# Optimization experiments

Measured on AMD Instinct MI355X. Metric: run time of the kernel, lower is better.

## Reference

```python
import jax, jax.numpy as jnp
import numpy as np

B, D = 128, 16384
EPS = 0.05
MAX_DEPTH = 5
D_MAX = 1000.0


def setup_inputs() -> dict:
    key = jax.random.key(0)
    k1, k2 = jax.random.split(key)
    theta = jax.random.normal(k1, (B, D), dtype=jnp.float32)
    prec = jax.random.uniform(k2, (D,), dtype=jnp.float32)
    return {"theta": theta, "prec": prec}


def _energy(theta, prec):
    # per-chain potential energy U(theta): [B]
    return 0.5 * jnp.einsum('bd,d,bd->b', theta, prec, theta)


def _grad_energy(theta, prec):
    # mirrors torch autograd.grad(energy.sum(), theta)
    return jax.grad(lambda th: _energy(th, prec).sum())(theta)


def _bdot(a, b):
    return jnp.einsum('bd,bd->b', a, b)


def _leapfrog(theta, r, prec, eps):
    gU = _grad_energy(theta, prec)
    r = r - 0.5 * eps * gU
    theta = theta + eps * r
    e = _energy(theta, prec)
    gU = _grad_energy(theta, prec)
    r = r - 0.5 * eps * gU
    return theta, r, e


def _buildtree(theta, r, u, eps_dir, j, key, prec):
    # returns (theta_near, r_near, theta_far, r_far, theta_prop, n, s)
    if j == 0:
        th, rp, e = _leapfrog(theta, r, prec, eps_dir)
        H = e + 0.5 * _bdot(rp, rp)
        n_p = (u <= jnp.exp(-H)).astype(jnp.int32)
        s_p = (jnp.log(u) - D_MAX < -H).astype(jnp.int32)
        return th, rp, th, rp, th, n_p, s_p
    k1, k2, k3 = jax.random.split(key, 3)
    th_n, r_n, th_f, r_f, th_p, n_p, s_p = _buildtree(theta, r, u, eps_dir, j - 1, k1, prec)
    _, _, th_f2, r_f2, th_pp, n_pp, s_pp = _buildtree(th_f, r_f, u, eps_dir, j - 1, k2, prec)
    # accept proposal from second subtree with prob n'' / (n' + n''), masked by s'
    denom = jnp.maximum(n_p + n_pp, 1).astype(jnp.float32)
    flag = (jax.random.uniform(k3, n_p.shape) < n_pp.astype(jnp.float32) / denom) & (s_p >= 1)
    th_p = jnp.where(flag[:, None], th_pp, th_p)
    # u-turn check; v*(far - near) == theta_plus - theta_minus
    v = jnp.sign(eps_dir)
    d = th_f2 - th_n
    s_new = (s_p * s_pp
             * ((v * _bdot(d, r_n)) >= 0.0).astype(jnp.int32)
             * ((v * _bdot(d, r_f2)) >= 0.0).astype(jnp.int32))
    n_new = n_p + jnp.where(s_p >= 1, n_pp, 0)
    return th_n, r_n, th_f2, r_f2, th_p, n_new, s_new


def _sample_trajectory(theta0, prec, key):
    kr, ku, key = jax.random.split(key, 3)
    r0 = jax.random.normal(kr, theta0.shape, theta0.dtype)
    H0 = _energy(theta0, prec) + 0.5 * _bdot(r0, r0)
    u = jax.random.uniform(ku, H0.shape, theta0.dtype) * jnp.exp(-H0)
    theta_r = theta0
    theta_f = theta0
    r_r = r0
    r_f = r0
    theta_m = theta0
    n = jnp.ones((theta0.shape[0],), jnp.int32)
    s = jnp.ones((theta0.shape[0],), jnp.int32)
    for j in range(MAX_DEPTH):  # tree doubling, bounded depth (jit-friendly)
        key, kv, kt, ka = jax.random.split(key, 4)
        v = jnp.where(jax.random.normal(kv, ()) >= 0.0, 1.0, -1.0)
        neg = v < 0.0
        st_th = jnp.where(neg, theta_r, theta_f)
        st_r = jnp.where(neg, r_r, r_f)
        _, _, th_far, r_far, th_p, n_p, s_p = _buildtree(st_th, st_r, u, v * EPS, j, kt, prec)
        theta_r = jnp.where(neg, th_far, theta_r)
        r_r = jnp.where(neg, r_far, r_r)
        theta_f = jnp.where(neg, theta_f, th_far)
        r_f = jnp.where(neg, r_f, r_far)
        acc = jax.random.uniform(ka, n.shape) < jnp.minimum(
            n_p.astype(jnp.float32) / n.astype(jnp.float32), 1.0)
        acc = acc & (s >= 1) & (s_p >= 1)
        theta_m = jnp.where(acc[:, None], th_p, theta_m)
        n = n + jnp.where(s >= 1, n_p, 0)
        d = theta_f - theta_r
        s = (s * s_p
             * (_bdot(d, r_r) >= 0.0).astype(jnp.int32)
             * (_bdot(d, r_f) >= 0.0).astype(jnp.int32))
    return theta_m


def reference(theta, prec):
    return _sample_trajectory(theta, prec, jax.random.key(42))
```

## Files before the change

### kernel.cpp

```cpp
#include <hip/hip_runtime.h>
#include <cstdint>
#include <cstring>


#define PARTITIONABLE 1

constexpr int NCHAIN = 128;
constexpr int NDIM   = 16384;
constexpr int VD     = 4;
constexpr int TPB    = 256;
constexpr int WGPC   = NDIM / (TPB * VD);
constexpr int NW     = NDIM / (64 * VD);
constexpr int NSLOT  = 62;
constexpr int NNODE  = 26;
constexpr float EPS  = 0.05f;

static_assert(NDIM % (TPB * VD) == 0, "tiling");

__host__ __device__ static inline void tf2(uint32_t k0, uint32_t k1,
                                           uint32_t x0, uint32_t x1,
                                           uint32_t& o0, uint32_t& o1) {
  const uint32_t ks2 = k0 ^ k1 ^ 0x1BD11BDAu;
  x0 += k0; x1 += k1;
#define TF_R(r) { x0 += x1; x1 = (x1 << (r)) | (x1 >> (32 - (r))); x1 ^= x0; }
  TF_R(13) TF_R(15) TF_R(26) TF_R(6)
  x0 += k1;  x1 += ks2 + 1u;
  TF_R(17) TF_R(29) TF_R(16) TF_R(24)
  x0 += ks2; x1 += k0 + 2u;
  TF_R(13) TF_R(15) TF_R(26) TF_R(6)
  x0 += k0;  x1 += k1 + 3u;
  TF_R(17) TF_R(29) TF_R(16) TF_R(24)
  x0 += k1;  x1 += ks2 + 4u;
  TF_R(13) TF_R(15) TF_R(26) TF_R(6)
  x0 += ks2; x1 += k0 + 5u;
#undef TF_R
  o0 = x0; o1 = x1;
}

__device__ static inline float u01(uint32_t bits) {
  return __uint_as_float((bits >> 9) | 0x3f800000u) - 1.0f;
}

__device__ static inline float erfinv32(float x) {
  float w = -log1pf(-x * x);
  float p;
  if (w < 5.0f) {
    w -= 2.5f;
    p = 2.81022636e-08f;
    p = fmaf(p, w, 3.43273939e-07f);
    p = fmaf(p, w, -3.5233877e-06f);
    p = fmaf(p, w, -4.39150654e-06f);
    p = fmaf(p, w, 0.00021858087f);
    p = fmaf(p, w, -0.00125372503f);
    p = fmaf(p, w, -0.00417768164f);
    p = fmaf(p, w, 0.246640727f);
    p = fmaf(p, w, 1.50140941f);
  } else {
    w = sqrtf(w) - 3.0f;
    p = -0.000200214257f;
    p = fmaf(p, w, 0.000100950558f);
    p = fmaf(p, w, 0.00134934322f);
    p = fmaf(p, w, -0.00367342844f);
    p = fmaf(p, w, 0.00573950773f);
    p = fmaf(p, w, -0.0076224613f);
    p = fmaf(p, w, 0.00943887047f);
    p = fmaf(p, w, 1.00167406f);
    p = fmaf(p, w, 2.83297682f);
  }
  return p * x;
}

__device__ static inline float norm_from_bits(uint32_t bits) {
  const float lo = __uint_as_float(0xBF7FFFFFu);
  float u = fmaxf(lo, fmaf(u01(bits), 2.0f, lo));
  return __uint_as_float(0x3FB504F3u) * erfinv32(u);
}

__device__ static inline float r0_elem(uint32_t k0, uint32_t k1, uint32_t i) {
#if PARTITIONABLE
  uint32_t a, c; tf2(k0, k1, 0u, i, a, c);
  return norm_from_bits(a ^ c);
#else
  const uint32_t H = (uint32_t)(NCHAIN * NDIM / 2);
  uint32_t a, c;
  if (i < H) { tf2(k0, k1, i, i + H, a, c); return norm_from_bits(a); }
  else       { tf2(k0, k1, i - H, i, a, c); return norm_from_bits(c); }
#endif
}

__device__ static inline float unif_chain(uint32_t k0, uint32_t k1, int b) {
#if PARTITIONABLE
  uint32_t a, c; tf2(k0, k1, 0u, (uint32_t)b, a, c);
  return u01(a ^ c);
#else
  uint32_t a, c;
  if (b < 64) { tf2(k0, k1, (uint32_t)b, (uint32_t)(b + 64), a, c); return u01(a); }
  else        { tf2(k0, k1, (uint32_t)(b - 64), (uint32_t)b, a, c); return u01(c); }
#endif
}

#define DPP_ADD(x, ctrl, rm)                                                   \
  (x) += __int_as_float(__builtin_amdgcn_update_dpp(                           \
      0, __float_as_int(x), (ctrl), (rm), 0xf, true));

__device__ static inline float wave_sum63(float x) {
  DPP_ADD(x, 0x111, 0xf)
  DPP_ADD(x, 0x112, 0xf)
  DPP_ADD(x, 0x114, 0xf)
  DPP_ADD(x, 0x118, 0xf)
  DPP_ADD(x, 0x142, 0xa)
  DPP_ADD(x, 0x143, 0xc)
  return x;
}

struct TrajParams { int v[5]; };
struct K2Params {
  uint32_t nk0[NNODE], nk1[NNODE];
  uint32_t ak0[5], ak1[5];
  int v[5];
};

template <int MODE>
__launch_bounds__(TPB, 4)
__global__ void k_traj(const float* __restrict__ th0g, const float* __restrict__ precg,
                       uint32_t kr0, uint32_t kr1,
                       float* __restrict__ partials,
                       const int* __restrict__ selg, float* __restrict__ outg,
                       TrajParams P) {
  const int chain   = blockIdx.x / WGPC;
  const int sblk    = blockIdx.x % WGPC;
  const int dimBase = sblk * (TPB * VD) + threadIdx.x * VD;
  const int lane    = threadIdx.x & 63;
  const int wv      = sblk * (TPB / 64) + (threadIdx.x >> 6);
  const uint32_t flat = (uint32_t)chain * NDIM + dimBase;

  float tha[VD], ra[VD], tho[VD], ro[VD], pc[VD];
  {
    const float4 t = *reinterpret_cast<const float4*>(th0g + (size_t)chain * NDIM + dimBase);
    const float4 p = *reinterpret_cast<const float4*>(precg + dimBase);
    tha[0]=t.x; tha[1]=t.y; tha[2]=t.z; tha[3]=t.w;
    pc [0]=p.x; pc [1]=p.y; pc [2]=p.z; pc [3]=p.w;
  }
#pragma unroll
  for (int d = 0; d < VD; ++d) ra[d] = r0_elem(kr0, kr1, flat + (uint32_t)d);
#pragma unroll
  for (int d = 0; d < VD; ++d) { tho[d] = tha[d]; ro[d] = ra[d]; }

  float near_t[5][VD], near_r[5][VD];
  float outv[VD];
  int selv = -2;
  if (MODE == 1) {
    selv = selg[chain];
#pragma unroll
    for (int d = 0; d < VD; ++d) outv[d] = tha[d];
  }

  int slot = 0, g = 0;
  bool cur_fwd = true;

#pragma unroll
  for (int j = 0; j < 5; ++j) {
    const bool fwd = P.v[j] > 0;
    if (fwd != cur_fwd) {
#pragma unroll
      for (int d = 0; d < VD; ++d) {
        float t;
        t = tha[d]; tha[d] = tho[d]; tho[d] = t;
        t = ra[d];  ra[d]  = ro[d];  ro[d]  = t;
      }
    }
    cur_fwd = fwd;
    const float e  = fwd ? EPS : -EPS;
    const float he = 0.5f * e;
    const int NL = 1 << j;
#pragma unroll
    for (int i = 0; i < NL; ++i) {
#pragma unroll
      for (int d = 0; d < VD; ++d) {
        float g1 = pc[d] * tha[d];
        ra[d]  = fmaf(-he, g1, ra[d]);
        tha[d] = fmaf(e, ra[d], tha[d]);
        float g2 = pc[d] * tha[d];
        ra[d]  = fmaf(-he, g2, ra[d]);
      }
      if (MODE == 1) {
        if (g == selv) {
#pragma unroll
          for (int d = 0; d < VD; ++d) outv[d] = tha[d];
        }
      }
      g++;
      if (MODE == 0) {
        const int p = __builtin_popcount((unsigned)i);
#pragma unroll
        for (int d = 0; d < VD; ++d) { near_t[p][d] = tha[d]; near_r[p][d] = ra[d]; }
        const int m = __builtin_ctz(~(unsigned)i);
#pragma unroll
        for (int k = 0; k < m; ++k) {
          const int s1 = p - 1 - k;
          float d1 = 0.f, d2 = 0.f;
#pragma unroll
          for (int d = 0; d < VD; ++d) {
            float dd = tha[d] - near_t[s1][d];
            d1 = fmaf(dd, near_r[s1][d], d1);
            d2 = fmaf(dd, ra[d], d2);
          }
          d1 = wave_sum63(d1);
          d2 = wave_sum63(d2);
          if (lane == 63) {
            partials[((size_t)(slot    ) * NCHAIN + chain) * NW + wv] = d1;
            partials[((size_t)(slot + 1) * NCHAIN + chain) * NW + wv] = d2;
          }
          slot += 2;
        }
      }
    }
    if (MODE == 0) {
      float p1 = 0.f, p2 = 0.f;
#pragma unroll
      for (int d = 0; d < VD; ++d) {
        float dd = tha[d] - tho[d];
        p1 = fmaf(dd, ra[d], p1);
        p2 = fmaf(dd, ro[d], p2);
      }
      p1 = wave_sum63(p1);
      p2 = wave_sum63(p2);
      if (lane == 63) {
        partials[((size_t)(slot    ) * NCHAIN + chain) * NW + wv] = p1;
        partials[((size_t)(slot + 1) * NCHAIN + chain) * NW + wv] = p2;
      }
      slot += 2;
    }
  }
  if (MODE == 1) {
    float4 o; o.x = outv[0]; o.y = outv[1]; o.z = outv[2]; o.w = outv[3];
    *reinterpret_cast<float4*>(outg + (size_t)chain * NDIM + dimBase) = o;
  }
}

__global__ void k_red(const float* __restrict__ partials, float* __restrict__ dots) {
  int w    = (blockIdx.x * blockDim.x + threadIdx.x) >> 6;
  int lane = threadIdx.x & 63;
  if (w >= NSLOT * NCHAIN) return;
  float v = partials[(size_t)w * NW + lane];
  v = wave_sum63(v);
  if (lane == 63) dots[w] = v;
}

__global__ void k_logic(const float* __restrict__ dots, int* __restrict__ selg,
                        K2Params P) {
  int b = threadIdx.x;
  if (b >= NCHAIN) return;
  int n = 1, s = 1, sel = -1;
  int slot = 0, nodeidx = 0, g = 0;
  int st_n[6], st_s[6], st_p[6];
  for (int j = 0; j < 5; ++j) {
    float vj = (P.v[j] > 0) ? 1.0f : -1.0f;
    int sp = 0;
    int NL = 1 << j;
    for (int i = 0; i < NL; ++i) {
      st_n[sp] = 1; st_s[sp] = 1; st_p[sp] = g; sp++; g++;
      int m = __builtin_ctz(~(unsigned)i);
      for (int k = 0; k < m; ++k) {
        int n1 = st_n[sp-2], s1 = st_s[sp-2], p1i = st_p[sp-2];
        int n2 = st_n[sp-1], s2 = st_s[sp-1], p2i = st_p[sp-1];
        float d1 = dots[(size_t)(slot    ) * NCHAIN + b];
        float d2 = dots[(size_t)(slot + 1) * NCHAIN + b];
        slot += 2;
        float uu = unif_chain(P.nk0[nodeidx], P.nk1[nodeidx], b);
        nodeidx++;
        int   dn    = n1 + n2; if (dn < 1) dn = 1;
        bool  flag  = (uu < (float)n2 / (float)dn) && (s1 >= 1);
        int   pm    = flag ? p2i : p1i;
        int   sm    = (s1 != 0 && s2 != 0 &&
                       (vj * d1 >= 0.0f) && (vj * d2 >= 0.0f)) ? 1 : 0;
        int   nm    = n1 + ((s1 >= 1) ? n2 : 0);
        st_n[sp-2] = nm; st_s[sp-2] = sm; st_p[sp-2] = pm;
        sp--;
      }
    }
    int n_p = st_n[0], s_p = st_s[0], th_p = st_p[0];
    float q1 = dots[(size_t)(slot    ) * NCHAIN + b];
    float q2 = dots[(size_t)(slot + 1) * NCHAIN + b];
    slot += 2;
    float dm1, dm2;
    if (P.v[j] > 0) { dm1 = q2;  dm2 = q1; }
    else            { dm1 = -q1; dm2 = -q2; }
    float au = unif_chain(P.ak0[j], P.ak1[j], b);
    float ratio = fminf((float)n_p / (float)n, 1.0f);
    bool acc = (au < ratio) && (s >= 1) && (s_p >= 1);
    if (acc) sel = th_p;
    n = n + ((s >= 1) ? n_p : 0);
    s = (s != 0 && s_p != 0 && (dm1 >= 0.0f) && (dm2 >= 0.0f)) ? 1 : 0;
  }
  selg[b] = sel;
}

static inline float host_bits_to_f(uint32_t fb) { float f; std::memcpy(&f, &fb, 4); return f; }

static void host_split(uint32_t k0, uint32_t k1, int nsub, uint32_t* o0, uint32_t* o1) {
#if PARTITIONABLE
  for (int i = 0; i < nsub; ++i) tf2(k0, k1, 0u, (uint32_t)i, o0[i], o1[i]);
#else
  uint32_t A[8], C[8], flat[16];
  for (int i = 0; i < nsub; ++i) tf2(k0, k1, (uint32_t)i, (uint32_t)(nsub + i), A[i], C[i]);
  for (int i = 0; i < nsub; ++i) { flat[i] = A[i]; flat[nsub + i] = C[i]; }
  for (int j = 0; j < nsub; ++j) { o0[j] = flat[2*j]; o1[j] = flat[2*j + 1]; }
#endif
}

static int host_vsign(uint32_t k0, uint32_t k1) {
  uint32_t a, c; tf2(k0, k1, 0u, 0u, a, c);
#if PARTITIONABLE
  uint32_t bits = a ^ c;
#else
  uint32_t bits = a;
#endif
  float f  = host_bits_to_f((bits >> 9) | 0x3f800000u) - 1.0f;
  float lo = host_bits_to_f(0xBF7FFFFFu);
  float u  = f * 2.0f + lo;
  return (u >= 0.0f) ? 1 : -1;
}

static void gen_nodes(uint32_t k0, uint32_t k1, int j,
                      uint32_t* nk0, uint32_t* nk1, int& idx) {
  if (j == 0) return;
  uint32_t o0[3], o1[3];
  host_split(k0, k1, 3, o0, o1);
  gen_nodes(o0[0], o1[0], j - 1, nk0, nk1, idx);
  gen_nodes(o0[1], o1[1], j - 1, nk0, nk1, idx);
  nk0[idx] = o0[2]; nk1[idx] = o1[2]; idx++;
}

extern "C" void kernel_launch(void* const* d_in, const int* in_sizes, int n_in,
                              void* d_out, int out_size, void* d_ws, size_t ws_size,
                              hipStream_t stream) {
  const float* th0  = (const float*)d_in[0];
  const float* prec = (const float*)d_in[1];
  float* out = (float*)d_out;

  float* partials = (float*)d_ws;
  float* dots     = partials + (size_t)NSLOT * NCHAIN * NW;
  int*   sel      = (int*)(dots + (size_t)NSLOT * NCHAIN);

  uint32_t key0 = 0u, key1 = 42u;
  uint32_t s0[4], s1[4];
  host_split(key0, key1, 3, s0, s1);
  const uint32_t kr0 = s0[0], kr1 = s1[0];
  key0 = s0[2]; key1 = s1[2];

  K2Params P2; TrajParams PT;
  int idx = 0;
  for (int j = 0; j < 5; ++j) {
    host_split(key0, key1, 4, s0, s1);
    key0 = s0[0]; key1 = s1[0];
    int v = host_vsign(s0[1], s1[1]);
    P2.v[j] = v; PT.v[j] = v;
    gen_nodes(s0[2], s1[2], j, P2.nk0, P2.nk1, idx);
    P2.ak0[j] = s0[3]; P2.ak1[j] = s1[3];
  }

  k_traj<0><<<dim3(NCHAIN * WGPC), dim3(TPB), 0, stream>>>(
      th0, prec, kr0, kr1, partials, sel, out, PT);
  k_red<<<dim3((NSLOT * NCHAIN * 64) / TPB), dim3(TPB), 0, stream>>>(partials, dots);
  k_logic<<<dim3(1), dim3(NCHAIN), 0, stream>>>(dots, sel, P2);
  k_traj<1><<<dim3(NCHAIN * WGPC), dim3(TPB), 0, stream>>>(
      th0, prec, kr0, kr1, partials, sel, out, PT);
}
```

Measured before the change: 125.7 us.

## Fuse tree-logic into replay kernel, precompute uniforms in reduce, skip unneeded replay

Removes the single-block k_logic launch. The per-chain tree-selection logic is now recomputed redundantly in every block of the replay kernel, and the per-node uniform draws are produced in the reduction kernel. The first trajectory pass keeps its near-state stack in LDS instead of registers and no longer fully unrolls the loops, which lowers register pressure. The replay pass skips the leapfrog entirely when no proposal was accepted and exits early once the selected step is reached. In exchange, every block repeats the scalar logic, and LDS traffic replaces register storage.

```diff
diff --git a/kernel.cpp b/kernel.cpp
--- a/kernel.cpp
+++ b/kernel.cpp
@@ -13,6 +13,7 @@
 constexpr int NW     = NDIM / (64 * VD);
 constexpr int NSLOT  = 62;
 constexpr int NNODE  = 26;
+constexpr int NKEY   = NNODE + 5;
 constexpr float EPS  = 0.05f;
 
 static_assert(NDIM % (TPB * VD) == 0, "tiling");
@@ -114,24 +115,19 @@
 }
 
 struct TrajParams { int v[5]; };
-struct K2Params {
-  uint32_t nk0[NNODE], nk1[NNODE];
-  uint32_t ak0[5], ak1[5];
-  int v[5];
-};
-
-template <int MODE>
+struct KeyParams  { uint32_t k0[NKEY], k1[NKEY]; };
+
 __launch_bounds__(TPB, 4)
-__global__ void k_traj(const float* __restrict__ th0g, const float* __restrict__ precg,
-                       uint32_t kr0, uint32_t kr1,
-                       float* __restrict__ partials,
-                       const int* __restrict__ selg, float* __restrict__ outg,
-                       TrajParams P) {
+__global__ void k_traj0(const float* __restrict__ th0g, const float* __restrict__ precg,
+                        uint32_t kr0, uint32_t kr1,
+                        float* __restrict__ partials, TrajParams P) {
+  __shared__ float stk[5][2][VD][TPB];
+  const int tid     = threadIdx.x;
   const int chain   = blockIdx.x / WGPC;
   const int sblk    = blockIdx.x % WGPC;
-  const int dimBase = sblk * (TPB * VD) + threadIdx.x * VD;
-  const int lane    = threadIdx.x & 63;
-  const int wv      = sblk * (TPB / 64) + (threadIdx.x >> 6);
+  const int dimBase = sblk * (TPB * VD) + tid * VD;
+  const int lane    = tid & 63;
+  const int wv      = sblk * (TPB / 64) + (tid >> 6);
   const uint32_t flat = (uint32_t)chain * NDIM + dimBase;
 
   float tha[VD], ra[VD], tho[VD], ro[VD], pc[VD];
@@ -146,19 +142,9 @@
 #pragma unroll
   for (int d = 0; d < VD; ++d) { tho[d] = tha[d]; ro[d] = ra[d]; }
 
-  float near_t[5][VD], near_r[5][VD];
-  float outv[VD];
-  int selv = -2;
-  if (MODE == 1) {
-    selv = selg[chain];
-#pragma unroll
-    for (int d = 0; d < VD; ++d) outv[d] = tha[d];
-  }
-
-  int slot = 0, g = 0;
+  int slot = 0;
   bool cur_fwd = true;
 
-#pragma unroll
   for (int j = 0; j < 5; ++j) {
     const bool fwd = P.v[j] > 0;
     if (fwd != cur_fwd) {
@@ -173,127 +159,182 @@
     const float e  = fwd ? EPS : -EPS;
     const float he = 0.5f * e;
     const int NL = 1 << j;
-#pragma unroll
     for (int i = 0; i < NL; ++i) {
 #pragma unroll
       for (int d = 0; d < VD; ++d) {
-        float g1 = pc[d] * tha[d];
-        ra[d]  = fmaf(-he, g1, ra[d]);
+        ra[d]  = fmaf(-he, pc[d] * tha[d], ra[d]);
         tha[d] = fmaf(e, ra[d], tha[d]);
-        float g2 = pc[d] * tha[d];
-        ra[d]  = fmaf(-he, g2, ra[d]);
-      }
-      if (MODE == 1) {
-        if (g == selv) {
+        ra[d]  = fmaf(-he, pc[d] * tha[d], ra[d]);
+      }
+      const int p = __builtin_popcount((unsigned)i);
+#pragma unroll
+      for (int d = 0; d < VD; ++d) {
+        stk[p][0][d][tid] = tha[d];
+        stk[p][1][d][tid] = ra[d];
+      }
+      const int m = __builtin_ctz(~(unsigned)i);
+      for (int k = 0; k < m; ++k) {
+        const int s1 = p - 1 - k;
+        float d1 = 0.f, d2 = 0.f;
+#pragma unroll
+        for (int d = 0; d < VD; ++d) {
+          float tn = stk[s1][0][d][tid];
+          float rn = stk[s1][1][d][tid];
+          float dd = tha[d] - tn;
+          d1 = fmaf(dd, rn, d1);
+          d2 = fmaf(dd, ra[d], d2);
+        }
+        d1 = wave_sum63(d1);
+        d2 = wave_sum63(d2);
+        if (lane == 63) {
+          partials[((size_t)(slot    ) * NCHAIN + chain) * NW + wv] = d1;
+          partials[((size_t)(slot + 1) * NCHAIN + chain) * NW + wv] = d2;
+        }
+        slot += 2;
+      }
+    }
+    float p1 = 0.f, p2 = 0.f;
+#pragma unroll
+    for (int d = 0; d < VD; ++d) {
+      float dd = tha[d] - tho[d];
+      p1 = fmaf(dd, ra[d], p1);
+      p2 = fmaf(dd, ro[d], p2);
+    }
+    p1 = wave_sum63(p1);
+    p2 = wave_sum63(p2);
+    if (lane == 63) {
+      partials[((size_t)(slot    ) * NCHAIN + chain) * NW + wv] = p1;
+      partials[((size_t)(slot + 1) * NCHAIN + chain) * NW + wv] = p2;
+    }
+    slot += 2;
+  }
+}
+
+__global__ void k_red(const float* __restrict__ partials, float* __restrict__ dots,
+                      float* __restrict__ unifs, KeyParams P) {
+  int gid  = blockIdx.x * blockDim.x + threadIdx.x;
+  int w    = gid >> 6;
+  int lane = gid & 63;
+  if (w < NSLOT * NCHAIN) {
+    float v = partials[(size_t)w * NW + lane];
+    v = wave_sum63(v);
+    if (lane == 63) dots[w] = v;
+  }
+  if (gid < NKEY * NCHAIN) {
+    int key = gid >> 7, b = gid & 127;
+    unifs[gid] = unif_chain(P.k0[key], P.k1[key], b);
+  }
+}
+
+__launch_bounds__(TPB, 4)
+__global__ void k_traj1(const float* __restrict__ th0g, const float* __restrict__ precg,
+                        uint32_t kr0, uint32_t kr1,
+                        const float* __restrict__ dots, const float* __restrict__ unifs,
+                        float* __restrict__ outg, TrajParams P) {
+  const int chain   = blockIdx.x / WGPC;
+  const int sblk    = blockIdx.x % WGPC;
+  const int dimBase = sblk * (TPB * VD) + threadIdx.x * VD;
+  const uint32_t flat = (uint32_t)chain * NDIM + dimBase;
+
+  int sel = -1;
+  {
+    int n = 1, s = 1;
+    int slot = 0, nodeidx = 0, g = 0;
+    int st_n[6], st_s[6], st_p[6];
+#pragma unroll
+    for (int j = 0; j < 5; ++j) {
+      const float vj = (P.v[j] > 0) ? 1.0f : -1.0f;
+      const int NL = 1 << j;
+      int sp = 0;
+#pragma unroll
+      for (int i = 0; i < NL; ++i) {
+        st_n[sp] = 1; st_s[sp] = 1; st_p[sp] = g; sp++; g++;
+        const int m = __builtin_ctz(~(unsigned)i);
+#pragma unroll
+        for (int k = 0; k < m; ++k) {
+          int n1 = st_n[sp-2], s1 = st_s[sp-2], p1i = st_p[sp-2];
+          int n2 = st_n[sp-1], s2 = st_s[sp-1], p2i = st_p[sp-1];
+          float d1 = dots[(size_t)(slot    ) * NCHAIN + chain];
+          float d2 = dots[(size_t)(slot + 1) * NCHAIN + chain];
+          slot += 2;
+          float uu = unifs[(size_t)nodeidx * NCHAIN + chain];
+          nodeidx++;
+          int  dn   = n1 + n2; if (dn < 1) dn = 1;
+          bool flag = (uu < (float)n2 / (float)dn) && (s1 >= 1);
+          int  pm   = flag ? p2i : p1i;
+          int  sm   = (s1 != 0 && s2 != 0 &&
+                       (vj * d1 >= 0.0f) && (vj * d2 >= 0.0f)) ? 1 : 0;
+          int  nm   = n1 + ((s1 >= 1) ? n2 : 0);
+          st_n[sp-2] = nm; st_s[sp-2] = sm; st_p[sp-2] = pm;
+          sp--;
+        }
+      }
+      int n_p = st_n[0], s_p = st_s[0], th_p = st_p[0];
+      float q1 = dots[(size_t)(slot    ) * NCHAIN + chain];
+      float q2 = dots[(size_t)(slot + 1) * NCHAIN + chain];
+      slot += 2;
+      float dm1, dm2;
+      if (P.v[j] > 0) { dm1 = q2;  dm2 = q1; }
+      else            { dm1 = -q1; dm2 = -q2; }
+      float au = unifs[(size_t)(NNODE + j) * NCHAIN + chain];
+      float ratio = fminf((float)n_p / (float)n, 1.0f);
+      bool acc = (au < ratio) && (s >= 1) && (s_p >= 1);
+      if (acc) sel = th_p;
+      n = n + ((s >= 1) ? n_p : 0);
+      s = (s != 0 && s_p != 0 && (dm1 >= 0.0f) && (dm2 >= 0.0f)) ? 1 : 0;
+    }
+  }
+
+  float tha[VD], ra[VD], tho[VD], ro[VD], pc[VD], outv[VD];
+  {
+    const float4 t = *reinterpret_cast<const float4*>(th0g + (size_t)chain * NDIM + dimBase);
+    const float4 p = *reinterpret_cast<const float4*>(precg + dimBase);
+    tha[0]=t.x; tha[1]=t.y; tha[2]=t.z; tha[3]=t.w;
+    pc [0]=p.x; pc [1]=p.y; pc [2]=p.z; pc [3]=p.w;
+  }
+#pragma unroll
+  for (int d = 0; d < VD; ++d) outv[d] = tha[d];
+  if (sel >= 0) {
+#pragma unroll
+    for (int d = 0; d < VD; ++d) ra[d] = r0_elem(kr0, kr1, flat + (uint32_t)d);
+#pragma unroll
+    for (int d = 0; d < VD; ++d) { tho[d] = tha[d]; ro[d] = ra[d]; }
+    int g = 0;
+    bool cur_fwd = true;
+    bool done = false;
+    for (int j = 0; j < 5 && !done; ++j) {
+      const bool fwd = P.v[j] > 0;
+      if (fwd != cur_fwd) {
+#pragma unroll
+        for (int d = 0; d < VD; ++d) {
+          float t;
+          t = tha[d]; tha[d] = tho[d]; tho[d] = t;
+          t = ra[d];  ra[d]  = ro[d];  ro[d]  = t;
+        }
+      }
+      cur_fwd = fwd;
+      const float e  = fwd ? EPS : -EPS;
+      const float he = 0.5f * e;
+      const int NL = 1 << j;
+      for (int i = 0; i < NL; ++i) {
+#pragma unroll
+        for (int d = 0; d < VD; ++d) {
+          ra[d]  = fmaf(-he, pc[d] * tha[d], ra[d]);
+          tha[d] = fmaf(e, ra[d], tha[d]);
+          ra[d]  = fmaf(-he, pc[d] * tha[d], ra[d]);
+        }
+        if (g == sel) {
 #pragma unroll
           for (int d = 0; d < VD; ++d) outv[d] = tha[d];
-        }
-      }
-      g++;
-      if (MODE == 0) {
-        const int p = __builtin_popcount((unsigned)i);
-#pragma unroll
-        for (int d = 0; d < VD; ++d) { near_t[p][d] = tha[d]; near_r[p][d] = ra[d]; }
-        const int m = __builtin_ctz(~(unsigned)i);
-#pragma unroll
-        for (int k = 0; k < m; ++k) {
-          const int s1 = p - 1 - k;
-          float d1 = 0.f, d2 = 0.f;
-#pragma unroll
-          for (int d = 0; d < VD; ++d) {
-            float dd = tha[d] - near_t[s1][d];
-            d1 = fmaf(dd, near_r[s1][d], d1);
-            d2 = fmaf(dd, ra[d], d2);
-          }
-          d1 = wave_sum63(d1);
-          d2 = wave_sum63(d2);
-          if (lane == 63) {
-            partials[((size_t)(slot    ) * NCHAIN + chain) * NW + wv] = d1;
-            partials[((size_t)(slot + 1) * NCHAIN + chain) * NW + wv] = d2;
-          }
-          slot += 2;
-        }
-      }
-    }
-    if (MODE == 0) {
-      float p1 = 0.f, p2 = 0.f;
-#pragma unroll
-      for (int d = 0; d < VD; ++d) {
-        float dd = tha[d] - tho[d];
-        p1 = fmaf(dd, ra[d], p1);
-        p2 = fmaf(dd, ro[d], p2);
-      }
-      p1 = wave_sum63(p1);
-      p2 = wave_sum63(p2);
-      if (lane == 63) {
-        partials[((size_t)(slot    ) * NCHAIN + chain) * NW + wv] = p1;
-        partials[((size_t)(slot + 1) * NCHAIN + chain) * NW + wv] = p2;
-      }
-      slot += 2;
-    }
-  }
-  if (MODE == 1) {
-    float4 o; o.x = outv[0]; o.y = outv[1]; o.z = outv[2]; o.w = outv[3];
-    *reinterpret_cast<float4*>(outg + (size_t)chain * NDIM + dimBase) = o;
-  }
-}
-
-__global__ void k_red(const float* __restrict__ partials, float* __restrict__ dots) {
-  int w    = (blockIdx.x * blockDim.x + threadIdx.x) >> 6;
-  int lane = threadIdx.x & 63;
-  if (w >= NSLOT * NCHAIN) return;
-  float v = partials[(size_t)w * NW + lane];
-  v = wave_sum63(v);
-  if (lane == 63) dots[w] = v;
-}
-
-__global__ void k_logic(const float* __restrict__ dots, int* __restrict__ selg,
-                        K2Params P) {
-  int b = threadIdx.x;
-  if (b >= NCHAIN) return;
-  int n = 1, s = 1, sel = -1;
-  int slot = 0, nodeidx = 0, g = 0;
-  int st_n[6], st_s[6], st_p[6];
-  for (int j = 0; j < 5; ++j) {
-    float vj = (P.v[j] > 0) ? 1.0f : -1.0f;
-    int sp = 0;
-    int NL = 1 << j;
-    for (int i = 0; i < NL; ++i) {
-      st_n[sp] = 1; st_s[sp] = 1; st_p[sp] = g; sp++; g++;
-      int m = __builtin_ctz(~(unsigned)i);
-      for (int k = 0; k < m; ++k) {
-        int n1 = st_n[sp-2], s1 = st_s[sp-2], p1i = st_p[sp-2];
-        int n2 = st_n[sp-1], s2 = st_s[sp-1], p2i = st_p[sp-1];
-        float d1 = dots[(size_t)(slot    ) * NCHAIN + b];
-        float d2 = dots[(size_t)(slot + 1) * NCHAIN + b];
-        slot += 2;
-        float uu = unif_chain(P.nk0[nodeidx], P.nk1[nodeidx], b);
-        nodeidx++;
-        int   dn    = n1 + n2; if (dn < 1) dn = 1;
-        bool  flag  = (uu < (float)n2 / (float)dn) && (s1 >= 1);
-        int   pm    = flag ? p2i : p1i;
-        int   sm    = (s1 != 0 && s2 != 0 &&
-                       (vj * d1 >= 0.0f) && (vj * d2 >= 0.0f)) ? 1 : 0;
-        int   nm    = n1 + ((s1 >= 1) ? n2 : 0);
-        st_n[sp-2] = nm; st_s[sp-2] = sm; st_p[sp-2] = pm;
-        sp--;
-      }
-    }
-    int n_p = st_n[0], s_p = st_s[0], th_p = st_p[0];
-    float q1 = dots[(size_t)(slot    ) * NCHAIN + b];
-    float q2 = dots[(size_t)(slot + 1) * NCHAIN + b];
-    slot += 2;
-    float dm1, dm2;
-    if (P.v[j] > 0) { dm1 = q2;  dm2 = q1; }
-    else            { dm1 = -q1; dm2 = -q2; }
-    float au = unif_chain(P.ak0[j], P.ak1[j], b);
-    float ratio = fminf((float)n_p / (float)n, 1.0f);
-    bool acc = (au < ratio) && (s >= 1) && (s_p >= 1);
-    if (acc) sel = th_p;
-    n = n + ((s >= 1) ? n_p : 0);
-    s = (s != 0 && s_p != 0 && (dm1 >= 0.0f) && (dm2 >= 0.0f)) ? 1 : 0;
-  }
-  selg[b] = sel;
+          done = true;
+          break;
+        }
+        g++;
+      }
+    }
+  }
+  float4 o; o.x = outv[0]; o.y = outv[1]; o.z = outv[2]; o.w = outv[3];
+  *reinterpret_cast<float4*>(outg + (size_t)chain * NDIM + dimBase) = o;
 }
 
 static inline float host_bits_to_f(uint32_t fb) { float f; std::memcpy(&f, &fb, 4); return f; }
@@ -341,7 +382,7 @@
 
   float* partials = (float*)d_ws;
   float* dots     = partials + (size_t)NSLOT * NCHAIN * NW;
-  int*   sel      = (int*)(dots + (size_t)NSLOT * NCHAIN);
+  float* unifs    = dots + (size_t)NSLOT * NCHAIN;
 
   uint32_t key0 = 0u, key1 = 42u;
   uint32_t s0[4], s1[4];
@@ -349,21 +390,20 @@
   const uint32_t kr0 = s0[0], kr1 = s1[0];
   key0 = s0[2]; key1 = s1[2];
 
-  K2Params P2; TrajParams PT;
+  KeyParams PK; TrajParams PT;
   int idx = 0;
   for (int j = 0; j < 5; ++j) {
     host_split(key0, key1, 4, s0, s1);
     key0 = s0[0]; key1 = s1[0];
-    int v = host_vsign(s0[1], s1[1]);
-    P2.v[j] = v; PT.v[j] = v;
-    gen_nodes(s0[2], s1[2], j, P2.nk0, P2.nk1, idx);
-    P2.ak0[j] = s0[3]; P2.ak1[j] = s1[3];
-  }
-
-  k_traj<0><<<dim3(NCHAIN * WGPC), dim3(TPB), 0, stream>>>(
-      th0, prec, kr0, kr1, partials, sel, out, PT);
-  k_red<<<dim3((NSLOT * NCHAIN * 64) / TPB), dim3(TPB), 0, stream>>>(partials, dots);
-  k_logic<<<dim3(1), dim3(NCHAIN), 0, stream>>>(dots, sel, P2);
-  k_traj<1><<<dim3(NCHAIN * WGPC), dim3(TPB), 0, stream>>>(
-      th0, prec, kr0, kr1, partials, sel, out, PT);
-}
+    PT.v[j] = host_vsign(s0[1], s1[1]);
+    gen_nodes(s0[2], s1[2], j, PK.k0, PK.k1, idx);
+    PK.k0[NNODE + j] = s0[3]; PK.k1[NNODE + j] = s1[3];
+  }
+
+  k_traj0<<<dim3(NCHAIN * WGPC), dim3(TPB), 0, stream>>>(
+      th0, prec, kr0, kr1, partials, PT);
+  k_red<<<dim3((NSLOT * NCHAIN * 64) / TPB), dim3(TPB), 0, stream>>>(
+      partials, dots, unifs, PK);
+  k_traj1<<<dim3(NCHAIN * WGPC), dim3(TPB), 0, stream>>>(
+      th0, prec, kr0, kr1, dots, unifs, out, PT);
+}
```

Measured after the change: 129.9 us. +3.3%, slower.

## Split trajectory kernel into template-unrolled pass and early-exit gather kernel

Applied to the files above, without the earlier changes.

The first trajectory pass is rewritten with compile-time template recursion over leaves, so popcount and ctz indices into the near-state arrays are constants and stay in registers. Its launch bound drops to 2 waves per EU. The second pass becomes a dedicated gather kernel that skips the r0 RNG and leapfrog work when no proposal was accepted, and stops integrating once the selected leaf is reached. The k_red lane index now comes from the global thread id. The cost is larger unrolled code and possibly lower occupancy.

```diff
diff --git a/kernel.cpp b/kernel.cpp
--- a/kernel.cpp
+++ b/kernel.cpp
@@ -120,127 +120,122 @@
   int v[5];
 };
 
-template <int MODE>
-__launch_bounds__(TPB, 4)
-__global__ void k_traj(const float* __restrict__ th0g, const float* __restrict__ precg,
-                       uint32_t kr0, uint32_t kr1,
-                       float* __restrict__ partials,
-                       const int* __restrict__ selg, float* __restrict__ outg,
-                       TrajParams P) {
+struct St {
+  float tha[VD], ra[VD], tho[VD], ro[VD], pc[VD];
+  float nt[5][VD], nr[5][VD];
+};
+
+template <int J, int I>
+__device__ __forceinline__ void leaf_body(St& st, const float e, const float he,
+                                          float* __restrict__ partials,
+                                          const int chain, const int wv,
+                                          const int lane, int& slot) {
+#pragma unroll
+  for (int d = 0; d < VD; ++d) {
+    st.ra[d]  = fmaf(-he, st.pc[d] * st.tha[d], st.ra[d]);
+    st.tha[d] = fmaf(e, st.ra[d], st.tha[d]);
+    st.ra[d]  = fmaf(-he, st.pc[d] * st.tha[d], st.ra[d]);
+  }
+  constexpr int P = __builtin_popcount((unsigned)I);
+#pragma unroll
+  for (int d = 0; d < VD; ++d) { st.nt[P][d] = st.tha[d]; st.nr[P][d] = st.ra[d]; }
+  constexpr int M = __builtin_ctz(~(unsigned)I);
+#pragma unroll
+  for (int k = 0; k < M; ++k) {
+    const int s1 = P - 1 - k;
+    float d1 = 0.f, d2 = 0.f;
+#pragma unroll
+    for (int d = 0; d < VD; ++d) {
+      float dd = st.tha[d] - st.nt[s1][d];
+      d1 = fmaf(dd, st.nr[s1][d], d1);
+      d2 = fmaf(dd, st.ra[d], d2);
+    }
+    d1 = wave_sum63(d1);
+    d2 = wave_sum63(d2);
+    if (lane == 63) {
+      partials[((size_t)(slot    ) * NCHAIN + chain) * NW + wv] = d1;
+      partials[((size_t)(slot + 1) * NCHAIN + chain) * NW + wv] = d2;
+    }
+    slot += 2;
+  }
+}
+
+template <int J, int I>
+__device__ __forceinline__ void run_level(St& st, const float e, const float he,
+                                          float* __restrict__ partials,
+                                          const int chain, const int wv,
+                                          const int lane, int& slot) {
+  leaf_body<J, I>(st, e, he, partials, chain, wv, lane, slot);
+  if constexpr (I + 1 < (1 << J))
+    run_level<J, I + 1>(st, e, he, partials, chain, wv, lane, slot);
+}
+
+__launch_bounds__(TPB, 2)
+__global__ void k_traj0(const float* __restrict__ th0g, const float* __restrict__ precg,
+                        uint32_t kr0, uint32_t kr1,
+                        float* __restrict__ partials, TrajParams P) {
+  const int tid     = threadIdx.x;
   const int chain   = blockIdx.x / WGPC;
   const int sblk    = blockIdx.x % WGPC;
-  const int dimBase = sblk * (TPB * VD) + threadIdx.x * VD;
-  const int lane    = threadIdx.x & 63;
-  const int wv      = sblk * (TPB / 64) + (threadIdx.x >> 6);
+  const int dimBase = sblk * (TPB * VD) + tid * VD;
+  const int lane    = tid & 63;
+  const int wv      = sblk * (TPB / 64) + (tid >> 6);
   const uint32_t flat = (uint32_t)chain * NDIM + dimBase;
 
-  float tha[VD], ra[VD], tho[VD], ro[VD], pc[VD];
+  St st;
   {
     const float4 t = *reinterpret_cast<const float4*>(th0g + (size_t)chain * NDIM + dimBase);
     const float4 p = *reinterpret_cast<const float4*>(precg + dimBase);
-    tha[0]=t.x; tha[1]=t.y; tha[2]=t.z; tha[3]=t.w;
-    pc [0]=p.x; pc [1]=p.y; pc [2]=p.z; pc [3]=p.w;
-  }
-#pragma unroll
-  for (int d = 0; d < VD; ++d) ra[d] = r0_elem(kr0, kr1, flat + (uint32_t)d);
-#pragma unroll
-  for (int d = 0; d < VD; ++d) { tho[d] = tha[d]; ro[d] = ra[d]; }
-
-  float near_t[5][VD], near_r[5][VD];
-  float outv[VD];
-  int selv = -2;
-  if (MODE == 1) {
-    selv = selg[chain];
-#pragma unroll
-    for (int d = 0; d < VD; ++d) outv[d] = tha[d];
-  }
-
-  int slot = 0, g = 0;
+    st.tha[0]=t.x; st.tha[1]=t.y; st.tha[2]=t.z; st.tha[3]=t.w;
+    st.pc [0]=p.x; st.pc [1]=p.y; st.pc [2]=p.z; st.pc [3]=p.w;
+  }
+#pragma unroll
+  for (int d = 0; d < VD; ++d) st.ra[d] = r0_elem(kr0, kr1, flat + (uint32_t)d);
+#pragma unroll
+  for (int d = 0; d < VD; ++d) { st.tho[d] = st.tha[d]; st.ro[d] = st.ra[d]; }
+
+  int slot = 0;
   bool cur_fwd = true;
 
-#pragma unroll
-  for (int j = 0; j < 5; ++j) {
-    const bool fwd = P.v[j] > 0;
-    if (fwd != cur_fwd) {
-#pragma unroll
-      for (int d = 0; d < VD; ++d) {
-        float t;
-        t = tha[d]; tha[d] = tho[d]; tho[d] = t;
-        t = ra[d];  ra[d]  = ro[d];  ro[d]  = t;
-      }
-    }
-    cur_fwd = fwd;
-    const float e  = fwd ? EPS : -EPS;
-    const float he = 0.5f * e;
-    const int NL = 1 << j;
-#pragma unroll
-    for (int i = 0; i < NL; ++i) {
-#pragma unroll
-      for (int d = 0; d < VD; ++d) {
-        float g1 = pc[d] * tha[d];
-        ra[d]  = fmaf(-he, g1, ra[d]);
-        tha[d] = fmaf(e, ra[d], tha[d]);
-        float g2 = pc[d] * tha[d];
-        ra[d]  = fmaf(-he, g2, ra[d]);
-      }
-      if (MODE == 1) {
-        if (g == selv) {
-#pragma unroll
-          for (int d = 0; d < VD; ++d) outv[d] = tha[d];
-        }
-      }
-      g++;
-      if (MODE == 0) {
-        const int p = __builtin_popcount((unsigned)i);
-#pragma unroll
-        for (int d = 0; d < VD; ++d) { near_t[p][d] = tha[d]; near_r[p][d] = ra[d]; }
-        const int m = __builtin_ctz(~(unsigned)i);
-#pragma unroll
-        for (int k = 0; k < m; ++k) {
-          const int s1 = p - 1 - k;
-          float d1 = 0.f, d2 = 0.f;
-#pragma unroll
-          for (int d = 0; d < VD; ++d) {
-            float dd = tha[d] - near_t[s1][d];
-            d1 = fmaf(dd, near_r[s1][d], d1);
-            d2 = fmaf(dd, ra[d], d2);
-          }
-          d1 = wave_sum63(d1);
-          d2 = wave_sum63(d2);
-          if (lane == 63) {
-            partials[((size_t)(slot    ) * NCHAIN + chain) * NW + wv] = d1;
-            partials[((size_t)(slot + 1) * NCHAIN + chain) * NW + wv] = d2;
-          }
-          slot += 2;
-        }
-      }
-    }
-    if (MODE == 0) {
-      float p1 = 0.f, p2 = 0.f;
-#pragma unroll
-      for (int d = 0; d < VD; ++d) {
-        float dd = tha[d] - tho[d];
-        p1 = fmaf(dd, ra[d], p1);
-        p2 = fmaf(dd, ro[d], p2);
-      }
-      p1 = wave_sum63(p1);
-      p2 = wave_sum63(p2);
-      if (lane == 63) {
-        partials[((size_t)(slot    ) * NCHAIN + chain) * NW + wv] = p1;
-        partials[((size_t)(slot + 1) * NCHAIN + chain) * NW + wv] = p2;
-      }
-      slot += 2;
-    }
-  }
-  if (MODE == 1) {
-    float4 o; o.x = outv[0]; o.y = outv[1]; o.z = outv[2]; o.w = outv[3];
-    *reinterpret_cast<float4*>(outg + (size_t)chain * NDIM + dimBase) = o;
-  }
+#define LEVEL(J)                                                               \
+  {                                                                            \
+    const bool fwd = P.v[J] > 0;                                               \
+    if (fwd != cur_fwd) {                                                      \
+      _Pragma("unroll")                                                        \
+      for (int d = 0; d < VD; ++d) {                                           \
+        float t;                                                               \
+        t = st.tha[d]; st.tha[d] = st.tho[d]; st.tho[d] = t;                   \
+        t = st.ra[d];  st.ra[d]  = st.ro[d];  st.ro[d]  = t;                   \
+      }                                                                        \
+    }                                                                          \
+    cur_fwd = fwd;                                                             \
+    const float e  = fwd ? EPS : -EPS;                                         \
+    const float he = 0.5f * e;                                                 \
+    run_level<J, 0>(st, e, he, partials, chain, wv, lane, slot);               \
+    float p1 = 0.f, p2 = 0.f;                                                  \
+    _Pragma("unroll")                                                          \
+    for (int d = 0; d < VD; ++d) {                                             \
+      float dd = st.tha[d] - st.tho[d];                                        \
+      p1 = fmaf(dd, st.ra[d], p1);                                             \
+      p2 = fmaf(dd, st.ro[d], p2);                                             \
+    }                                                                          \
+    p1 = wave_sum63(p1);                                                       \
+    p2 = wave_sum63(p2);                                                       \
+    if (lane == 63) {                                                          \
+      partials[((size_t)(slot    ) * NCHAIN + chain) * NW + wv] = p1;          \
+      partials[((size_t)(slot + 1) * NCHAIN + chain) * NW + wv] = p2;          \
+    }                                                                          \
+    slot += 2;                                                                 \
+  }
+
+  LEVEL(0) LEVEL(1) LEVEL(2) LEVEL(3) LEVEL(4)
+#undef LEVEL
 }
 
 __global__ void k_red(const float* __restrict__ partials, float* __restrict__ dots) {
-  int w    = (blockIdx.x * blockDim.x + threadIdx.x) >> 6;
-  int lane = threadIdx.x & 63;
+  int gid  = blockIdx.x * blockDim.x + threadIdx.x;
+  int w    = gid >> 6;
+  int lane = gid & 63;
   if (w >= NSLOT * NCHAIN) return;
   float v = partials[(size_t)w * NW + lane];
   v = wave_sum63(v);
@@ -296,6 +291,69 @@
   selg[b] = sel;
 }
 
+__launch_bounds__(TPB, 2)
+__global__ void k_gather(const float* __restrict__ th0g, const float* __restrict__ precg,
+                         uint32_t kr0, uint32_t kr1,
+                         const int* __restrict__ selg, float* __restrict__ outg,
+                         TrajParams P) {
+  const int chain   = blockIdx.x / WGPC;
+  const int sblk    = blockIdx.x % WGPC;
+  const int dimBase = sblk * (TPB * VD) + threadIdx.x * VD;
+  const uint32_t flat = (uint32_t)chain * NDIM + dimBase;
+  const int sel = selg[chain];
+
+  float tha[VD], ra[VD], tho[VD], ro[VD], pc[VD], outv[VD];
+  {
+    const float4 t = *reinterpret_cast<const float4*>(th0g + (size_t)chain * NDIM + dimBase);
+    const float4 p = *reinterpret_cast<const float4*>(precg + dimBase);
+    tha[0]=t.x; tha[1]=t.y; tha[2]=t.z; tha[3]=t.w;
+    pc [0]=p.x; pc [1]=p.y; pc [2]=p.z; pc [3]=p.w;
+  }
+#pragma unroll
+  for (int d = 0; d < VD; ++d) outv[d] = tha[d];
+  if (sel >= 0) {
+#pragma unroll
+    for (int d = 0; d < VD; ++d) ra[d] = r0_elem(kr0, kr1, flat + (uint32_t)d);
+#pragma unroll
+    for (int d = 0; d < VD; ++d) { tho[d] = tha[d]; ro[d] = ra[d]; }
+    int g = 0;
+    bool cur_fwd = true;
+    bool done = false;
+    for (int j = 0; j < 5 && !done; ++j) {
+      const bool fwd = P.v[j] > 0;
+      if (fwd != cur_fwd) {
+#pragma unroll
+        for (int d = 0; d < VD; ++d) {
+          float t;
+          t = tha[d]; tha[d] = tho[d]; tho[d] = t;
+          t = ra[d];  ra[d]  = ro[d];  ro[d]  = t;
+        }
+      }
+      cur_fwd = fwd;
+      const float e  = fwd ? EPS : -EPS;
+      const float he = 0.5f * e;
+      const int NL = 1 << j;
+      for (int i = 0; i < NL; ++i) {
+#pragma unroll
+        for (int d = 0; d < VD; ++d) {
+          ra[d]  = fmaf(-he, pc[d] * tha[d], ra[d]);
+          tha[d] = fmaf(e, ra[d], tha[d]);
+          ra[d]  = fmaf(-he, pc[d] * tha[d], ra[d]);
+        }
+        if (g == sel) {
+#pragma unroll
+          for (int d = 0; d < VD; ++d) outv[d] = tha[d];
+          done = true;
+          break;
+        }
+        g++;
+      }
+    }
+  }
+  float4 o; o.x = outv[0]; o.y = outv[1]; o.z = outv[2]; o.w = outv[3];
+  *reinterpret_cast<float4*>(outg + (size_t)chain * NDIM + dimBase) = o;
+}
+
 static inline float host_bits_to_f(uint32_t fb) { float f; std::memcpy(&f, &fb, 4); return f; }
 
 static void host_split(uint32_t k0, uint32_t k1, int nsub, uint32_t* o0, uint32_t* o1) {
@@ -360,10 +418,10 @@
     P2.ak0[j] = s0[3]; P2.ak1[j] = s1[3];
   }
 
-  k_traj<0><<<dim3(NCHAIN * WGPC), dim3(TPB), 0, stream>>>(
-      th0, prec, kr0, kr1, partials, sel, out, PT);
+  k_traj0<<<dim3(NCHAIN * WGPC), dim3(TPB), 0, stream>>>(
+      th0, prec, kr0, kr1, partials, PT);
   k_red<<<dim3((NSLOT * NCHAIN * 64) / TPB), dim3(TPB), 0, stream>>>(partials, dots);
   k_logic<<<dim3(1), dim3(NCHAIN), 0, stream>>>(dots, sel, P2);
-  k_traj<1><<<dim3(NCHAIN * WGPC), dim3(TPB), 0, stream>>>(
-      th0, prec, kr0, kr1, partials, sel, out, PT);
-}
+  k_gather<<<dim3(NCHAIN * WGPC), dim3(TPB), 0, stream>>>(
+      th0, prec, kr0, kr1, sel, out, PT);
+}
```

Result: no change. 123.6 us (-1.7%).
